# Optimization experiments

Measured on AMD Instinct MI355X. Metric: run time of the kernel, lower is better.

## Reference

```python
import jax, jax.numpy as jnp
import numpy as np
from math import sqrt

IN_DIM = 512
OUT_DIM = 512
MOD_DIM = 256
BATCH = 1024
EPS = 1e-8


def _uniform_param(key, shape, fan_in):
    # torch.rand in [0,1) then scaled to [-k, k) with k = sqrt(1/fan_in)
    k = sqrt(1.0 / fan_in)
    return jax.random.uniform(key, shape, dtype=jnp.float32, minval=-k, maxval=k)


def setup_inputs() -> dict:
    key = jax.random.key(0)
    k1, k2, k3, k4, k5, k6 = jax.random.split(key, 6)
    modulations = jax.random.normal(k1, (BATCH, MOD_DIM), dtype=jnp.float32)
    x = jax.random.normal(k2, (BATCH, IN_DIM), dtype=jnp.float32)
    weight = _uniform_param(k3, (OUT_DIM, IN_DIM), IN_DIM)      # main weight
    bias = _uniform_param(k4, (OUT_DIM,), IN_DIM)               # main bias
    # nn.Linear(modulation_dim, in_dim): weight [in_dim, mod_dim], bias [in_dim]
    mod_w = _uniform_param(k5, (IN_DIM, MOD_DIM), MOD_DIM)
    mod_b = _uniform_param(k6, (IN_DIM,), MOD_DIM)
    return {"modulations": modulations, "x": x, "weight": weight,
            "bias": bias, "mod_w": mod_w, "mod_b": mod_b}


def reference(modulations, x, weight, bias, mod_w, mod_b):
    # scales: [B, in_dim]
    scales = modulations @ mod_w.T + mod_b
    # weight_1: [B, out_dim, in_dim] = weight broadcast-scaled per sample
    w1 = weight[None, :, :] * scales[:, None, :]
    # NOTE: faithful to source: sum over axis -2 (the OUT dim), per-column L2 renorm
    w2 = w1 * jax.lax.rsqrt(jnp.sum(jnp.square(w1), axis=-2, keepdims=True) + EPS)
    # (x.unsqueeze(-2) @ w2.transpose(-2,-1)).squeeze(-2) + bias -> [B, out_dim]
    out = jnp.einsum("bi,boi->bo", x, w2) + bias
    return out
```

## Files before the change

### kernel.cpp

```cpp
#include <hip/hip_runtime.h>
#include <math.h>

#define B_DIM    1024
#define IN_DIMS  512
#define OUT_DIMS 512
#define MOD_DIM  256
#define EPS_F    1e-8f
#define SP       72

typedef __attribute__((ext_vector_type(8))) short bf16x8;
typedef __attribute__((ext_vector_type(4))) float f32x4;

__device__ __forceinline__ unsigned short f2bf(float f) {
    union { float f; unsigned u; } c; c.f = f;
    unsigned r = c.u + 0x7fffu + ((c.u >> 16) & 1u);
    return (unsigned short)(r >> 16);
}
__device__ __forceinline__ float bf2f(unsigned short h) {
    union { float f; unsigned u; } c; c.u = ((unsigned)h) << 16;
    return c.f;
}

__global__ __launch_bounds__(256) void prep_w(
    const float* __restrict__ weight, float* __restrict__ colsum,
    unsigned short* __restrict__ w_bf)
{
    __shared__ float4 sm[16][16];
    const int q = threadIdx.x & 15;
    const int r = threadIdx.x >> 4;
    const int col = blockIdx.x * 64 + q * 4;
    float4 acc = {0.f, 0.f, 0.f, 0.f};
    #pragma unroll
    for (int it = 0; it < 32; it++) {
        const int row = r + 16 * it;
        float4 v = *(const float4*)&weight[row * IN_DIMS + col];
        acc.x += v.x * v.x; acc.y += v.y * v.y;
        acc.z += v.z * v.z; acc.w += v.w * v.w;
        ushort4 h;
        h.x = f2bf(v.x); h.y = f2bf(v.y); h.z = f2bf(v.z); h.w = f2bf(v.w);
        *(ushort4*)&w_bf[row * IN_DIMS + col] = h;
    }
    sm[r][q] = acc;
    __syncthreads();
    if (threadIdx.x < 16) {
        float4 s = sm[0][threadIdx.x];
        #pragma unroll
        for (int j = 1; j < 16; j++) {
            float4 v = sm[j][threadIdx.x];
            s.x += v.x; s.y += v.y; s.z += v.z; s.w += v.w;
        }
        *(float4*)&colsum[blockIdx.x * 64 + threadIdx.x * 4] = s;
    }
}

__global__ __launch_bounds__(256) void gemm_mod(
    const float* __restrict__ A,
    const float* __restrict__ Bw,
    const float* __restrict__ mod_b,
    const float* __restrict__ x,
    const float* __restrict__ colsum,
    unsigned short* __restrict__ t_bf)
{
    __shared__ unsigned short Ah[64 * SP], Al[64 * SP], Bh[64 * SP], Bl[64 * SP];
    const int tid = threadIdx.x;
    const int m0 = blockIdx.y * 64, n0 = blockIdx.x * 64;
    const int lane = tid & 63, wv = tid >> 6;
    const int wm = (wv >> 1) * 32, wn = (wv & 1) * 32;
    const int lr = lane & 15, lq = lane >> 4;

    f32x4 acc[2][2] = {};

    for (int kt = 0; kt < MOD_DIM; kt += 64) {
        #pragma unroll
        for (int i = 0; i < 4; i++) {
            const int idx = tid + i * 256;
            const int r  = idx >> 4;
            const int k4 = (idx & 15) * 4;
            float4 va = *(const float4*)&A[(m0 + r) * MOD_DIM + kt + k4];
            ushort4 h, l;
            h.x = f2bf(va.x); l.x = f2bf(va.x - bf2f(h.x));
            h.y = f2bf(va.y); l.y = f2bf(va.y - bf2f(h.y));
            h.z = f2bf(va.z); l.z = f2bf(va.z - bf2f(h.z));
            h.w = f2bf(va.w); l.w = f2bf(va.w - bf2f(h.w));
            *(ushort4*)&Ah[r * SP + k4] = h;
            *(ushort4*)&Al[r * SP + k4] = l;
            float4 vb = *(const float4*)&Bw[(n0 + r) * MOD_DIM + kt + k4];
            h.x = f2bf(vb.x); l.x = f2bf(vb.x - bf2f(h.x));
            h.y = f2bf(vb.y); l.y = f2bf(vb.y - bf2f(h.y));
            h.z = f2bf(vb.z); l.z = f2bf(vb.z - bf2f(h.z));
            h.w = f2bf(vb.w); l.w = f2bf(vb.w - bf2f(h.w));
            *(ushort4*)&Bh[r * SP + k4] = h;
            *(ushort4*)&Bl[r * SP + k4] = l;
        }
        __syncthreads();

        #pragma unroll
        for (int kk = 0; kk < 64; kk += 32) {
            const int ko = kk + lq * 8;
            bf16x8 ah0 = *(bf16x8*)&Ah[(wm +      lr) * SP + ko];
            bf16x8 ah1 = *(bf16x8*)&Ah[(wm + 16 + lr) * SP + ko];
            bf16x8 al0 = *(bf16x8*)&Al[(wm +      lr) * SP + ko];
            bf16x8 al1 = *(bf16x8*)&Al[(wm + 16 + lr) * SP + ko];
            bf16x8 bh0 = *(bf16x8*)&Bh[(wn +      lr) * SP + ko];
            bf16x8 bh1 = *(bf16x8*)&Bh[(wn + 16 + lr) * SP + ko];
            bf16x8 bl0 = *(bf16x8*)&Bl[(wn +      lr) * SP + ko];
            bf16x8 bl1 = *(bf16x8*)&Bl[(wn + 16 + lr) * SP + ko];
            acc[0][0] = __builtin_amdgcn_mfma_f32_16x16x32_bf16(ah0, bh0, acc[0][0], 0, 0, 0);
            acc[0][1] = __builtin_amdgcn_mfma_f32_16x16x32_bf16(ah0, bh1, acc[0][1], 0, 0, 0);
            acc[1][0] = __builtin_amdgcn_mfma_f32_16x16x32_bf16(ah1, bh0, acc[1][0], 0, 0, 0);
            acc[1][1] = __builtin_amdgcn_mfma_f32_16x16x32_bf16(ah1, bh1, acc[1][1], 0, 0, 0);
            acc[0][0] = __builtin_amdgcn_mfma_f32_16x16x32_bf16(ah0, bl0, acc[0][0], 0, 0, 0);
            acc[0][1] = __builtin_amdgcn_mfma_f32_16x16x32_bf16(ah0, bl1, acc[0][1], 0, 0, 0);
            acc[1][0] = __builtin_amdgcn_mfma_f32_16x16x32_bf16(ah1, bl0, acc[1][0], 0, 0, 0);
            acc[1][1] = __builtin_amdgcn_mfma_f32_16x16x32_bf16(ah1, bl1, acc[1][1], 0, 0, 0);
            acc[0][0] = __builtin_amdgcn_mfma_f32_16x16x32_bf16(al0, bh0, acc[0][0], 0, 0, 0);
            acc[0][1] = __builtin_amdgcn_mfma_f32_16x16x32_bf16(al0, bh1, acc[0][1], 0, 0, 0);
            acc[1][0] = __builtin_amdgcn_mfma_f32_16x16x32_bf16(al1, bh0, acc[1][0], 0, 0, 0);
            acc[1][1] = __builtin_amdgcn_mfma_f32_16x16x32_bf16(al1, bh1, acc[1][1], 0, 0, 0);
        }
        __syncthreads();
    }

    #pragma unroll
    for (int i = 0; i < 2; i++) {
        #pragma unroll
        for (int j = 0; j < 2; j++) {
            const int gn = n0 + wn + 16 * j + lr;
            const float cs = colsum[gn];
            const float mb = mod_b[gn];
            #pragma unroll
            for (int rr = 0; rr < 4; rr++) {
                const int gm = m0 + wm + 16 * i + lq * 4 + rr;
                const float s = acc[i][j][rr] + mb;
                const float tv = x[gm * IN_DIMS + gn] * s * rsqrtf(s * s * cs + EPS_F);
                t_bf[gm * IN_DIMS + gn] = f2bf(tv);
            }
        }
    }
}

__global__ __launch_bounds__(256) void gemm_out(
    const unsigned short* __restrict__ A,
    const unsigned short* __restrict__ Bw,
    const float* __restrict__ bias,
    float* __restrict__ out)
{
    __shared__ unsigned short As[64 * SP], Bs[64 * SP];
    const int tid = threadIdx.x;
    const int m0 = blockIdx.y * 64, n0 = blockIdx.x * 64;
    const int lane = tid & 63, wv = tid >> 6;
    const int wm = (wv >> 1) * 32, wn = (wv & 1) * 32;
    const int lr = lane & 15, lq = lane >> 4;

    f32x4 acc[2][2] = {};

    for (int kt = 0; kt < IN_DIMS; kt += 64) {
        #pragma unroll
        for (int i = 0; i < 2; i++) {
            const int idx = tid + i * 256;
            const int r  = idx >> 3;
            const int k8 = (idx & 7) * 8;
            *(uint4*)&As[r * SP + k8] = *(const uint4*)&A [(m0 + r) * IN_DIMS + kt + k8];
            *(uint4*)&Bs[r * SP + k8] = *(const uint4*)&Bw[(n0 + r) * IN_DIMS + kt + k8];
        }
        __syncthreads();

        #pragma unroll
        for (int kk = 0; kk < 64; kk += 32) {
            const int ko = kk + lq * 8;
            bf16x8 a0 = *(bf16x8*)&As[(wm +      lr) * SP + ko];
            bf16x8 a1 = *(bf16x8*)&As[(wm + 16 + lr) * SP + ko];
            bf16x8 b0 = *(bf16x8*)&Bs[(wn +      lr) * SP + ko];
            bf16x8 b1 = *(bf16x8*)&Bs[(wn + 16 + lr) * SP + ko];
            acc[0][0] = __builtin_amdgcn_mfma_f32_16x16x32_bf16(a0, b0, acc[0][0], 0, 0, 0);
            acc[0][1] = __builtin_amdgcn_mfma_f32_16x16x32_bf16(a0, b1, acc[0][1], 0, 0, 0);
            acc[1][0] = __builtin_amdgcn_mfma_f32_16x16x32_bf16(a1, b0, acc[1][0], 0, 0, 0);
            acc[1][1] = __builtin_amdgcn_mfma_f32_16x16x32_bf16(a1, b1, acc[1][1], 0, 0, 0);
        }
        __syncthreads();
    }

    #pragma unroll
    for (int i = 0; i < 2; i++) {
        #pragma unroll
        for (int j = 0; j < 2; j++) {
            const int gn = n0 + wn + 16 * j + lr;
            const float bv = bias[gn];
            #pragma unroll
            for (int rr = 0; rr < 4; rr++) {
                const int gm = m0 + wm + 16 * i + lq * 4 + rr;
                out[gm * OUT_DIMS + gn] = acc[i][j][rr] + bv;
            }
        }
    }
}

extern "C" void kernel_launch(void* const* d_in, const int* in_sizes, int n_in,
                              void* d_out, int out_size, void* d_ws, size_t ws_size,
                              hipStream_t stream)
{
    const float* modulations = (const float*)d_in[0];
    const float* x           = (const float*)d_in[1];
    const float* weight      = (const float*)d_in[2];
    const float* bias        = (const float*)d_in[3];
    const float* mod_w       = (const float*)d_in[4];
    const float* mod_b       = (const float*)d_in[5];
    float* out = (float*)d_out;

    char* wsb = (char*)d_ws;
    float* colsum         = (float*)wsb;
    unsigned short* w_bf  = (unsigned short*)(wsb + 4096);
    unsigned short* t_bf  = (unsigned short*)(wsb + 4096 + 524288);

    prep_w<<<IN_DIMS / 64, 256, 0, stream>>>(weight, colsum, w_bf);

    gemm_mod<<<dim3(IN_DIMS / 64, B_DIM / 64), 256, 0, stream>>>(
        modulations, mod_w, mod_b, x, colsum, t_bf);

    gemm_out<<<dim3(OUT_DIMS / 64, B_DIM / 64), 256, 0, stream>>>(
        t_bf, w_bf, bias, out);
}
```

Measured before the change: 91.58 us.

## Presplit modulation operands in prep kernel and stage GEMM tiles in two large K chunks

The prep kernel now also splits mod_w and modulations into bf16 hi/lo arrays once, so gemm_mod no longer converts fp32 to split bf16 in every tile. Both GEMMs now load K in two halves: the first half goes to LDS, and the second half is prefetched into registers while the first is computed. This cuts the number of barriers and overlaps global loads with MFMA work. The cost is larger LDS use (64KB in gemm_mod, 64KB in gemm_out), unpadded row strides that may cause bank conflicts, more workspace traffic, and higher register pressure that may lower occupancy.

New measurement: 99.96 us. 1.09x slower.

```diff
diff --git a/kernel.cpp b/kernel.cpp
--- a/kernel.cpp
+++ b/kernel.cpp
@@ -6,7 +6,6 @@
 #define OUT_DIMS 512
 #define MOD_DIM  256
 #define EPS_F    1e-8f
-#define SP       72
 
 typedef __attribute__((ext_vector_type(8))) short bf16x8;
 typedef __attribute__((ext_vector_type(4))) float f32x4;
@@ -20,91 +19,139 @@
     union { float f; unsigned u; } c; c.u = ((unsigned)h) << 16;
     return c.f;
 }
-
-__global__ __launch_bounds__(256) void prep_w(
-    const float* __restrict__ weight, float* __restrict__ colsum,
-    unsigned short* __restrict__ w_bf)
-{
-    __shared__ float4 sm[16][16];
-    const int q = threadIdx.x & 15;
-    const int r = threadIdx.x >> 4;
-    const int col = blockIdx.x * 64 + q * 4;
-    float4 acc = {0.f, 0.f, 0.f, 0.f};
-    #pragma unroll
-    for (int it = 0; it < 32; it++) {
-        const int row = r + 16 * it;
-        float4 v = *(const float4*)&weight[row * IN_DIMS + col];
-        acc.x += v.x * v.x; acc.y += v.y * v.y;
-        acc.z += v.z * v.z; acc.w += v.w * v.w;
-        ushort4 h;
-        h.x = f2bf(v.x); h.y = f2bf(v.y); h.z = f2bf(v.z); h.w = f2bf(v.w);
-        *(ushort4*)&w_bf[row * IN_DIMS + col] = h;
-    }
-    sm[r][q] = acc;
-    __syncthreads();
-    if (threadIdx.x < 16) {
-        float4 s = sm[0][threadIdx.x];
-        #pragma unroll
-        for (int j = 1; j < 16; j++) {
-            float4 v = sm[j][threadIdx.x];
-            s.x += v.x; s.y += v.y; s.z += v.z; s.w += v.w;
-        }
-        *(float4*)&colsum[blockIdx.x * 64 + threadIdx.x * 4] = s;
+__device__ __forceinline__ void split4(float4 v, ushort4& h, ushort4& l) {
+    h.x = f2bf(v.x); l.x = f2bf(v.x - bf2f(h.x));
+    h.y = f2bf(v.y); l.y = f2bf(v.y - bf2f(h.y));
+    h.z = f2bf(v.z); l.z = f2bf(v.z - bf2f(h.z));
+    h.w = f2bf(v.w); l.w = f2bf(v.w - bf2f(h.w));
+}
+
+__global__ __launch_bounds__(256) void prep(
+    const float* __restrict__ weight, const float* __restrict__ mod_w,
+    const float* __restrict__ mods,
+    float* __restrict__ colsum, unsigned short* __restrict__ w_bf,
+    unsigned short* __restrict__ mwh, unsigned short* __restrict__ mwl,
+    unsigned short* __restrict__ mh,  unsigned short* __restrict__ ml)
+{
+    const int b = blockIdx.x, tid = threadIdx.x;
+    if (b < 8) {
+        __shared__ float4 sm[16][16];
+        const int q = tid & 15, r = tid >> 4;
+        const int col = b * 64 + q * 4;
+        float4 acc = {0.f, 0.f, 0.f, 0.f};
+        #pragma unroll
+        for (int it = 0; it < 32; it++) {
+            const int row = r + 16 * it;
+            float4 v = *(const float4*)&weight[row * IN_DIMS + col];
+            acc.x += v.x * v.x; acc.y += v.y * v.y;
+            acc.z += v.z * v.z; acc.w += v.w * v.w;
+            ushort4 h;
+            h.x = f2bf(v.x); h.y = f2bf(v.y); h.z = f2bf(v.z); h.w = f2bf(v.w);
+            *(ushort4*)&w_bf[row * IN_DIMS + col] = h;
+        }
+        sm[r][q] = acc;
+        __syncthreads();
+        if (tid < 16) {
+            float4 s = sm[0][tid];
+            #pragma unroll
+            for (int j = 1; j < 16; j++) {
+                float4 v = sm[j][tid];
+                s.x += v.x; s.y += v.y; s.z += v.z; s.w += v.w;
+            }
+            *(float4*)&colsum[b * 64 + tid * 4] = s;
+        }
+    } else if (b < 16) {
+        const int rb = b - 8;
+        #pragma unroll
+        for (int i = 0; i < 16; i++) {
+            const int id = tid + i * 256;
+            const int r = rb * 64 + (id >> 6);
+            const int c = (id & 63) * 4;
+            float4 v = *(const float4*)&mod_w[r * MOD_DIM + c];
+            ushort4 h, l; split4(v, h, l);
+            *(ushort4*)&mwh[r * MOD_DIM + c] = h;
+            *(ushort4*)&mwl[r * MOD_DIM + c] = l;
+        }
+    } else {
+        const int rb = b - 16;
+        #pragma unroll
+        for (int i = 0; i < 8; i++) {
+            const int id = tid + i * 256;
+            const int r = rb * 32 + (id >> 6);
+            const int c = (id & 63) * 4;
+            float4 v = *(const float4*)&mods[r * MOD_DIM + c];
+            ushort4 h, l; split4(v, h, l);
+            *(ushort4*)&mh[r * MOD_DIM + c] = h;
+            *(ushort4*)&ml[r * MOD_DIM + c] = l;
+        }
     }
 }
 
 __global__ __launch_bounds__(256) void gemm_mod(
-    const float* __restrict__ A,
-    const float* __restrict__ Bw,
-    const float* __restrict__ mod_b,
-    const float* __restrict__ x,
-    const float* __restrict__ colsum,
-    unsigned short* __restrict__ t_bf)
-{
-    __shared__ unsigned short Ah[64 * SP], Al[64 * SP], Bh[64 * SP], Bl[64 * SP];
+    const unsigned short* __restrict__ Amh, const unsigned short* __restrict__ Aml,
+    const unsigned short* __restrict__ Bmh, const unsigned short* __restrict__ Bml,
+    const float* __restrict__ mod_b, const float* __restrict__ x,
+    const float* __restrict__ colsum, unsigned short* __restrict__ t_bf)
+{
+    __shared__ unsigned short Ah[64 * 128], Al[64 * 128], Bh[64 * 128], Bl[64 * 128];
     const int tid = threadIdx.x;
     const int m0 = blockIdx.y * 64, n0 = blockIdx.x * 64;
     const int lane = tid & 63, wv = tid >> 6;
     const int wm = (wv >> 1) * 32, wn = (wv & 1) * 32;
     const int lr = lane & 15, lq = lane >> 4;
 
+    int sr[4], sc[4];
+    #pragma unroll
+    for (int i = 0; i < 4; i++) { int id = tid + i * 256; sr[i] = id >> 4; sc[i] = (id & 15) * 8; }
+
+    uint4 gah[4], gal[4], gbh[4], gbl[4];
+    #pragma unroll
+    for (int i = 0; i < 4; i++) {
+        gah[i] = *(const uint4*)&Amh[(m0 + sr[i]) * MOD_DIM + sc[i]];
+        gal[i] = *(const uint4*)&Aml[(m0 + sr[i]) * MOD_DIM + sc[i]];
+        gbh[i] = *(const uint4*)&Bmh[(n0 + sr[i]) * MOD_DIM + sc[i]];
+        gbl[i] = *(const uint4*)&Bml[(n0 + sr[i]) * MOD_DIM + sc[i]];
+    }
+    #pragma unroll
+    for (int i = 0; i < 4; i++) {
+        *(uint4*)&Ah[sr[i] * 128 + sc[i]] = gah[i];
+        *(uint4*)&Al[sr[i] * 128 + sc[i]] = gal[i];
+        *(uint4*)&Bh[sr[i] * 128 + sc[i]] = gbh[i];
+        *(uint4*)&Bl[sr[i] * 128 + sc[i]] = gbl[i];
+    }
+    #pragma unroll
+    for (int i = 0; i < 4; i++) {
+        gah[i] = *(const uint4*)&Amh[(m0 + sr[i]) * MOD_DIM + 128 + sc[i]];
+        gal[i] = *(const uint4*)&Aml[(m0 + sr[i]) * MOD_DIM + 128 + sc[i]];
+        gbh[i] = *(const uint4*)&Bmh[(n0 + sr[i]) * MOD_DIM + 128 + sc[i]];
+        gbl[i] = *(const uint4*)&Bml[(n0 + sr[i]) * MOD_DIM + 128 + sc[i]];
+    }
+
     f32x4 acc[2][2] = {};
-
-    for (int kt = 0; kt < MOD_DIM; kt += 64) {
-        #pragma unroll
-        for (int i = 0; i < 4; i++) {
-            const int idx = tid + i * 256;
-            const int r  = idx >> 4;
-            const int k4 = (idx & 15) * 4;
-            float4 va = *(const float4*)&A[(m0 + r) * MOD_DIM + kt + k4];
-            ushort4 h, l;
-            h.x = f2bf(va.x); l.x = f2bf(va.x - bf2f(h.x));
-            h.y = f2bf(va.y); l.y = f2bf(va.y - bf2f(h.y));
-            h.z = f2bf(va.z); l.z = f2bf(va.z - bf2f(h.z));
-            h.w = f2bf(va.w); l.w = f2bf(va.w - bf2f(h.w));
-            *(ushort4*)&Ah[r * SP + k4] = h;
-            *(ushort4*)&Al[r * SP + k4] = l;
-            float4 vb = *(const float4*)&Bw[(n0 + r) * MOD_DIM + kt + k4];
-            h.x = f2bf(vb.x); l.x = f2bf(vb.x - bf2f(h.x));
-            h.y = f2bf(vb.y); l.y = f2bf(vb.y - bf2f(h.y));
-            h.z = f2bf(vb.z); l.z = f2bf(vb.z - bf2f(h.z));
-            h.w = f2bf(vb.w); l.w = f2bf(vb.w - bf2f(h.w));
-            *(ushort4*)&Bh[r * SP + k4] = h;
-            *(ushort4*)&Bl[r * SP + k4] = l;
-        }
+    #pragma unroll
+    for (int it = 0; it < 2; it++) {
         __syncthreads();
-
-        #pragma unroll
-        for (int kk = 0; kk < 64; kk += 32) {
+        if (it == 1) {
+            #pragma unroll
+            for (int i = 0; i < 4; i++) {
+                *(uint4*)&Ah[sr[i] * 128 + sc[i]] = gah[i];
+                *(uint4*)&Al[sr[i] * 128 + sc[i]] = gal[i];
+                *(uint4*)&Bh[sr[i] * 128 + sc[i]] = gbh[i];
+                *(uint4*)&Bl[sr[i] * 128 + sc[i]] = gbl[i];
+            }
+            __syncthreads();
+        }
+        #pragma unroll
+        for (int kk = 0; kk < 128; kk += 32) {
             const int ko = kk + lq * 8;
-            bf16x8 ah0 = *(bf16x8*)&Ah[(wm +      lr) * SP + ko];
-            bf16x8 ah1 = *(bf16x8*)&Ah[(wm + 16 + lr) * SP + ko];
-            bf16x8 al0 = *(bf16x8*)&Al[(wm +      lr) * SP + ko];
-            bf16x8 al1 = *(bf16x8*)&Al[(wm + 16 + lr) * SP + ko];
-            bf16x8 bh0 = *(bf16x8*)&Bh[(wn +      lr) * SP + ko];
-            bf16x8 bh1 = *(bf16x8*)&Bh[(wn + 16 + lr) * SP + ko];
-            bf16x8 bl0 = *(bf16x8*)&Bl[(wn +      lr) * SP + ko];
-            bf16x8 bl1 = *(bf16x8*)&Bl[(wn + 16 + lr) * SP + ko];
+            bf16x8 ah0 = *(bf16x8*)&Ah[(wm +      lr) * 128 + ko];
+            bf16x8 ah1 = *(bf16x8*)&Ah[(wm + 16 + lr) * 128 + ko];
+            bf16x8 al0 = *(bf16x8*)&Al[(wm +      lr) * 128 + ko];
+            bf16x8 al1 = *(bf16x8*)&Al[(wm + 16 + lr) * 128 + ko];
+            bf16x8 bh0 = *(bf16x8*)&Bh[(wn +      lr) * 128 + ko];
+            bf16x8 bh1 = *(bf16x8*)&Bh[(wn + 16 + lr) * 128 + ko];
+            bf16x8 bl0 = *(bf16x8*)&Bl[(wn +      lr) * 128 + ko];
+            bf16x8 bl1 = *(bf16x8*)&Bl[(wn + 16 + lr) * 128 + ko];
             acc[0][0] = __builtin_amdgcn_mfma_f32_16x16x32_bf16(ah0, bh0, acc[0][0], 0, 0, 0);
             acc[0][1] = __builtin_amdgcn_mfma_f32_16x16x32_bf16(ah0, bh1, acc[0][1], 0, 0, 0);
             acc[1][0] = __builtin_amdgcn_mfma_f32_16x16x32_bf16(ah1, bh0, acc[1][0], 0, 0, 0);
@@ -118,7 +165,6 @@
             acc[1][0] = __builtin_amdgcn_mfma_f32_16x16x32_bf16(al1, bh0, acc[1][0], 0, 0, 0);
             acc[1][1] = __builtin_amdgcn_mfma_f32_16x16x32_bf16(al1, bh1, acc[1][1], 0, 0, 0);
         }
-        __syncthreads();
     }
 
     #pragma unroll
@@ -142,42 +188,60 @@
 __global__ __launch_bounds__(256) void gemm_out(
     const unsigned short* __restrict__ A,
     const unsigned short* __restrict__ Bw,
-    const float* __restrict__ bias,
-    float* __restrict__ out)
-{
-    __shared__ unsigned short As[64 * SP], Bs[64 * SP];
+    const float* __restrict__ bias, float* __restrict__ out)
+{
+    __shared__ unsigned short As[64 * 256], Bs[64 * 256];
     const int tid = threadIdx.x;
     const int m0 = blockIdx.y * 64, n0 = blockIdx.x * 64;
     const int lane = tid & 63, wv = tid >> 6;
     const int wm = (wv >> 1) * 32, wn = (wv & 1) * 32;
     const int lr = lane & 15, lq = lane >> 4;
 
+    int sr[8], sc[8];
+    #pragma unroll
+    for (int i = 0; i < 8; i++) { int id = tid + i * 256; sr[i] = id >> 5; sc[i] = (id & 31) * 8; }
+
+    uint4 ga[8], gb[8];
+    #pragma unroll
+    for (int i = 0; i < 8; i++) {
+        ga[i] = *(const uint4*)&A [(m0 + sr[i]) * IN_DIMS + sc[i]];
+        gb[i] = *(const uint4*)&Bw[(n0 + sr[i]) * IN_DIMS + sc[i]];
+    }
+    #pragma unroll
+    for (int i = 0; i < 8; i++) {
+        *(uint4*)&As[sr[i] * 256 + sc[i]] = ga[i];
+        *(uint4*)&Bs[sr[i] * 256 + sc[i]] = gb[i];
+    }
+    #pragma unroll
+    for (int i = 0; i < 8; i++) {
+        ga[i] = *(const uint4*)&A [(m0 + sr[i]) * IN_DIMS + 256 + sc[i]];
+        gb[i] = *(const uint4*)&Bw[(n0 + sr[i]) * IN_DIMS + 256 + sc[i]];
+    }
+
     f32x4 acc[2][2] = {};
-
-    for (int kt = 0; kt < IN_DIMS; kt += 64) {
-        #pragma unroll
-        for (int i = 0; i < 2; i++) {
-            const int idx = tid + i * 256;
-            const int r  = idx >> 3;
-            const int k8 = (idx & 7) * 8;
-            *(uint4*)&As[r * SP + k8] = *(const uint4*)&A [(m0 + r) * IN_DIMS + kt + k8];
-            *(uint4*)&Bs[r * SP + k8] = *(const uint4*)&Bw[(n0 + r) * IN_DIMS + kt + k8];
-        }
+    #pragma unroll
+    for (int it = 0; it < 2; it++) {
         __syncthreads();
-
-        #pragma unroll
-        for (int kk = 0; kk < 64; kk += 32) {
+        if (it == 1) {
+            #pragma unroll
+            for (int i = 0; i < 8; i++) {
+                *(uint4*)&As[sr[i] * 256 + sc[i]] = ga[i];
+                *(uint4*)&Bs[sr[i] * 256 + sc[i]] = gb[i];
+            }
+            __syncthreads();
+        }
+        #pragma unroll
+        for (int kk = 0; kk < 256; kk += 32) {
             const int ko = kk + lq * 8;
-            bf16x8 a0 = *(bf16x8*)&As[(wm +      lr) * SP + ko];
-            bf16x8 a1 = *(bf16x8*)&As[(wm + 16 + lr) * SP + ko];
-            bf16x8 b0 = *(bf16x8*)&Bs[(wn +      lr) * SP + ko];
-            bf16x8 b1 = *(bf16x8*)&Bs[(wn + 16 + lr) * SP + ko];
+            bf16x8 a0 = *(bf16x8*)&As[(wm +      lr) * 256 + ko];
+            bf16x8 a1 = *(bf16x8*)&As[(wm + 16 + lr) * 256 + ko];
+            bf16x8 b0 = *(bf16x8*)&Bs[(wn +      lr) * 256 + ko];
+            bf16x8 b1 = *(bf16x8*)&Bs[(wn + 16 + lr) * 256 + ko];
             acc[0][0] = __builtin_amdgcn_mfma_f32_16x16x32_bf16(a0, b0, acc[0][0], 0, 0, 0);
             acc[0][1] = __builtin_amdgcn_mfma_f32_16x16x32_bf16(a0, b1, acc[0][1], 0, 0, 0);
             acc[1][0] = __builtin_amdgcn_mfma_f32_16x16x32_bf16(a1, b0, acc[1][0], 0, 0, 0);
             acc[1][1] = __builtin_amdgcn_mfma_f32_16x16x32_bf16(a1, b1, acc[1][1], 0, 0, 0);
         }
-        __syncthreads();
     }
 
     #pragma unroll
@@ -208,14 +272,19 @@
     float* out = (float*)d_out;
 
     char* wsb = (char*)d_ws;
-    float* colsum         = (float*)wsb;
-    unsigned short* w_bf  = (unsigned short*)(wsb + 4096);
-    unsigned short* t_bf  = (unsigned short*)(wsb + 4096 + 524288);
-
-    prep_w<<<IN_DIMS / 64, 256, 0, stream>>>(weight, colsum, w_bf);
+    float* colsum        = (float*)wsb;
+    unsigned short* w_bf = (unsigned short*)(wsb + 4096);
+    unsigned short* t_bf = (unsigned short*)(wsb + 4096 + 524288);
+    unsigned short* mwh  = (unsigned short*)(wsb + 4096 + 524288 + 1048576);
+    unsigned short* mwl  = (unsigned short*)(wsb + 4096 + 524288 + 1048576 + 262144);
+    unsigned short* mh   = (unsigned short*)(wsb + 4096 + 524288 + 1048576 + 524288);
+    unsigned short* ml   = (unsigned short*)(wsb + 4096 + 524288 + 1048576 + 524288 + 524288);
+
+    prep<<<48, 256, 0, stream>>>(weight, mod_w, modulations,
+                                 colsum, w_bf, mwh, mwl, mh, ml);
 
     gemm_mod<<<dim3(IN_DIMS / 64, B_DIM / 64), 256, 0, stream>>>(
-        modulations, mod_w, mod_b, x, colsum, t_bf);
+        mh, ml, mwh, mwl, mod_b, x, colsum, t_bf);
 
     gemm_out<<<dim3(OUT_DIMS / 64, B_DIM / 64), 256, 0, stream>>>(
         t_bf, w_bf, bias, out);
```

## Fold weight prep into both GEMM kernels and stage full-K tiles in LDS

Applied to the files above, without the earlier changes.

Removes the separate prep_w kernel. Each k1_mod block now recomputes its own column sums of weight, and k2_out converts fp32 weight to bf16 on the fly. Both GEMMs switch to 32x64 tiles, so each uses 256 blocks, and they load the whole K extent into LDS once instead of looping over K-tiles. This drops one launch and the workspace round trip for w_bf, at the cost of redundant weight reads (32x per column block), more LDS per block that may lower occupancy, and no overlap between loads and MFMA work.

After: 77.44 us. 15.4% less time.

```diff
diff --git a/kernel.cpp b/kernel.cpp
--- a/kernel.cpp
+++ b/kernel.cpp
@@ -6,7 +6,6 @@
 #define OUT_DIMS 512
 #define MOD_DIM  256
 #define EPS_F    1e-8f
-#define SP       72
 
 typedef __attribute__((ext_vector_type(8))) short bf16x8;
 typedef __attribute__((ext_vector_type(4))) float f32x4;
@@ -21,176 +20,166 @@
     return c.f;
 }
 
-__global__ __launch_bounds__(256) void prep_w(
-    const float* __restrict__ weight, float* __restrict__ colsum,
-    unsigned short* __restrict__ w_bf)
-{
-    __shared__ float4 sm[16][16];
-    const int q = threadIdx.x & 15;
-    const int r = threadIdx.x >> 4;
-    const int col = blockIdx.x * 64 + q * 4;
-    float4 acc = {0.f, 0.f, 0.f, 0.f};
-    #pragma unroll
-    for (int it = 0; it < 32; it++) {
-        const int row = r + 16 * it;
-        float4 v = *(const float4*)&weight[row * IN_DIMS + col];
-        acc.x += v.x * v.x; acc.y += v.y * v.y;
-        acc.z += v.z * v.z; acc.w += v.w * v.w;
-        ushort4 h;
-        h.x = f2bf(v.x); h.y = f2bf(v.y); h.z = f2bf(v.z); h.w = f2bf(v.w);
-        *(ushort4*)&w_bf[row * IN_DIMS + col] = h;
-    }
-    sm[r][q] = acc;
-    __syncthreads();
-    if (threadIdx.x < 16) {
-        float4 s = sm[0][threadIdx.x];
-        #pragma unroll
-        for (int j = 1; j < 16; j++) {
-            float4 v = sm[j][threadIdx.x];
-            s.x += v.x; s.y += v.y; s.z += v.z; s.w += v.w;
-        }
-        *(float4*)&colsum[blockIdx.x * 64 + threadIdx.x * 4] = s;
-    }
-}
-
-__global__ __launch_bounds__(256) void gemm_mod(
-    const float* __restrict__ A,
-    const float* __restrict__ Bw,
+#define LP1 264
+__global__ __launch_bounds__(256) void k1_mod(
+    const float* __restrict__ mods,
+    const float* __restrict__ mod_w,
     const float* __restrict__ mod_b,
+    const float* __restrict__ weight,
     const float* __restrict__ x,
-    const float* __restrict__ colsum,
     unsigned short* __restrict__ t_bf)
 {
-    __shared__ unsigned short Ah[64 * SP], Al[64 * SP], Bh[64 * SP], Bl[64 * SP];
+    __shared__ unsigned short Ah[32 * LP1], Al[32 * LP1];
+    __shared__ unsigned short Bh[64 * LP1], Bl[64 * LP1];
+    __shared__ float4 csm[16][16];
+    __shared__ float colsum_s[64];
+
     const int tid = threadIdx.x;
-    const int m0 = blockIdx.y * 64, n0 = blockIdx.x * 64;
+    const int n0 = blockIdx.x * 64;
+    const int m0 = blockIdx.y * 32;
     const int lane = tid & 63, wv = tid >> 6;
-    const int wm = (wv >> 1) * 32, wn = (wv & 1) * 32;
+    const int wm = (wv >> 1) * 16, wn = (wv & 1) * 32;
     const int lr = lane & 15, lq = lane >> 4;
 
-    f32x4 acc[2][2] = {};
-
-    for (int kt = 0; kt < MOD_DIM; kt += 64) {
-        #pragma unroll
-        for (int i = 0; i < 4; i++) {
-            const int idx = tid + i * 256;
-            const int r  = idx >> 4;
-            const int k4 = (idx & 15) * 4;
-            float4 va = *(const float4*)&A[(m0 + r) * MOD_DIM + kt + k4];
-            ushort4 h, l;
-            h.x = f2bf(va.x); l.x = f2bf(va.x - bf2f(h.x));
-            h.y = f2bf(va.y); l.y = f2bf(va.y - bf2f(h.y));
-            h.z = f2bf(va.z); l.z = f2bf(va.z - bf2f(h.z));
-            h.w = f2bf(va.w); l.w = f2bf(va.w - bf2f(h.w));
-            *(ushort4*)&Ah[r * SP + k4] = h;
-            *(ushort4*)&Al[r * SP + k4] = l;
-            float4 vb = *(const float4*)&Bw[(n0 + r) * MOD_DIM + kt + k4];
-            h.x = f2bf(vb.x); l.x = f2bf(vb.x - bf2f(h.x));
-            h.y = f2bf(vb.y); l.y = f2bf(vb.y - bf2f(h.y));
-            h.z = f2bf(vb.z); l.z = f2bf(vb.z - bf2f(h.z));
-            h.w = f2bf(vb.w); l.w = f2bf(vb.w - bf2f(h.w));
-            *(ushort4*)&Bh[r * SP + k4] = h;
-            *(ushort4*)&Bl[r * SP + k4] = l;
-        }
-        __syncthreads();
-
-        #pragma unroll
-        for (int kk = 0; kk < 64; kk += 32) {
-            const int ko = kk + lq * 8;
-            bf16x8 ah0 = *(bf16x8*)&Ah[(wm +      lr) * SP + ko];
-            bf16x8 ah1 = *(bf16x8*)&Ah[(wm + 16 + lr) * SP + ko];
-            bf16x8 al0 = *(bf16x8*)&Al[(wm +      lr) * SP + ko];
-            bf16x8 al1 = *(bf16x8*)&Al[(wm + 16 + lr) * SP + ko];
-            bf16x8 bh0 = *(bf16x8*)&Bh[(wn +      lr) * SP + ko];
-            bf16x8 bh1 = *(bf16x8*)&Bh[(wn + 16 + lr) * SP + ko];
-            bf16x8 bl0 = *(bf16x8*)&Bl[(wn +      lr) * SP + ko];
-            bf16x8 bl1 = *(bf16x8*)&Bl[(wn + 16 + lr) * SP + ko];
-            acc[0][0] = __builtin_amdgcn_mfma_f32_16x16x32_bf16(ah0, bh0, acc[0][0], 0, 0, 0);
-            acc[0][1] = __builtin_amdgcn_mfma_f32_16x16x32_bf16(ah0, bh1, acc[0][1], 0, 0, 0);
-            acc[1][0] = __builtin_amdgcn_mfma_f32_16x16x32_bf16(ah1, bh0, acc[1][0], 0, 0, 0);
-            acc[1][1] = __builtin_amdgcn_mfma_f32_16x16x32_bf16(ah1, bh1, acc[1][1], 0, 0, 0);
-            acc[0][0] = __builtin_amdgcn_mfma_f32_16x16x32_bf16(ah0, bl0, acc[0][0], 0, 0, 0);
-            acc[0][1] = __builtin_amdgcn_mfma_f32_16x16x32_bf16(ah0, bl1, acc[0][1], 0, 0, 0);
-            acc[1][0] = __builtin_amdgcn_mfma_f32_16x16x32_bf16(ah1, bl0, acc[1][0], 0, 0, 0);
-            acc[1][1] = __builtin_amdgcn_mfma_f32_16x16x32_bf16(ah1, bl1, acc[1][1], 0, 0, 0);
-            acc[0][0] = __builtin_amdgcn_mfma_f32_16x16x32_bf16(al0, bh0, acc[0][0], 0, 0, 0);
-            acc[0][1] = __builtin_amdgcn_mfma_f32_16x16x32_bf16(al0, bh1, acc[0][1], 0, 0, 0);
-            acc[1][0] = __builtin_amdgcn_mfma_f32_16x16x32_bf16(al1, bh0, acc[1][0], 0, 0, 0);
-            acc[1][1] = __builtin_amdgcn_mfma_f32_16x16x32_bf16(al1, bh1, acc[1][1], 0, 0, 0);
-        }
-        __syncthreads();
-    }
-
-    #pragma unroll
-    for (int i = 0; i < 2; i++) {
-        #pragma unroll
-        for (int j = 0; j < 2; j++) {
-            const int gn = n0 + wn + 16 * j + lr;
-            const float cs = colsum[gn];
-            const float mb = mod_b[gn];
-            #pragma unroll
-            for (int rr = 0; rr < 4; rr++) {
-                const int gm = m0 + wm + 16 * i + lq * 4 + rr;
-                const float s = acc[i][j][rr] + mb;
-                const float tv = x[gm * IN_DIMS + gn] * s * rsqrtf(s * s * cs + EPS_F);
-                t_bf[gm * IN_DIMS + gn] = f2bf(tv);
-            }
-        }
-    }
-}
-
-__global__ __launch_bounds__(256) void gemm_out(
-    const unsigned short* __restrict__ A,
-    const unsigned short* __restrict__ Bw,
+    #pragma unroll
+    for (int i = 0; i < 8; i++) {
+        const int id = tid + i * 256;
+        const int r = id >> 6, c4 = id & 63;
+        float4 v = *(const float4*)&mods[(m0 + r) * MOD_DIM + c4 * 4];
+        ushort4 h, l;
+        h.x = f2bf(v.x); l.x = f2bf(v.x - bf2f(h.x));
+        h.y = f2bf(v.y); l.y = f2bf(v.y - bf2f(h.y));
+        h.z = f2bf(v.z); l.z = f2bf(v.z - bf2f(h.z));
+        h.w = f2bf(v.w); l.w = f2bf(v.w - bf2f(h.w));
+        *(ushort4*)&Ah[r * LP1 + c4 * 4] = h;
+        *(ushort4*)&Al[r * LP1 + c4 * 4] = l;
+    }
+    #pragma unroll
+    for (int i = 0; i < 16; i++) {
+        const int id = tid + i * 256;
+        const int r = id >> 6, c4 = id & 63;
+        float4 v = *(const float4*)&mod_w[(n0 + r) * MOD_DIM + c4 * 4];
+        ushort4 h, l;
+        h.x = f2bf(v.x); l.x = f2bf(v.x - bf2f(h.x));
+        h.y = f2bf(v.y); l.y = f2bf(v.y - bf2f(h.y));
+        h.z = f2bf(v.z); l.z = f2bf(v.z - bf2f(h.z));
+        h.w = f2bf(v.w); l.w = f2bf(v.w - bf2f(h.w));
+        *(ushort4*)&Bh[r * LP1 + c4 * 4] = h;
+        *(ushort4*)&Bl[r * LP1 + c4 * 4] = l;
+    }
+
+    {
+        const int c4 = tid & 15, rr = tid >> 4;
+        float4 acc = {0.f, 0.f, 0.f, 0.f};
+        #pragma unroll
+        for (int it = 0; it < 32; it++) {
+            const int row = rr + 16 * it;
+            float4 v = *(const float4*)&weight[row * IN_DIMS + n0 + c4 * 4];
+            acc.x += v.x * v.x; acc.y += v.y * v.y;
+            acc.z += v.z * v.z; acc.w += v.w * v.w;
+        }
+        csm[rr][c4] = acc;
+    }
+    __syncthreads();
+    if (tid < 16) {
+        float4 s = csm[0][tid];
+        #pragma unroll
+        for (int j = 1; j < 16; j++) {
+            float4 v = csm[j][tid];
+            s.x += v.x; s.y += v.y; s.z += v.z; s.w += v.w;
+        }
+        *(float4*)&colsum_s[tid * 4] = s;
+    }
+
+    f32x4 acc[2] = {};
+    #pragma unroll
+    for (int kk = 0; kk < 256; kk += 32) {
+        const int ko = kk + lq * 8;
+        bf16x8 ah = *(bf16x8*)&Ah[(wm + lr) * LP1 + ko];
+        bf16x8 al = *(bf16x8*)&Al[(wm + lr) * LP1 + ko];
+        bf16x8 bh0 = *(bf16x8*)&Bh[(wn +      lr) * LP1 + ko];
+        bf16x8 bh1 = *(bf16x8*)&Bh[(wn + 16 + lr) * LP1 + ko];
+        bf16x8 bl0 = *(bf16x8*)&Bl[(wn +      lr) * LP1 + ko];
+        bf16x8 bl1 = *(bf16x8*)&Bl[(wn + 16 + lr) * LP1 + ko];
+        acc[0] = __builtin_amdgcn_mfma_f32_16x16x32_bf16(ah, bh0, acc[0], 0, 0, 0);
+        acc[1] = __builtin_amdgcn_mfma_f32_16x16x32_bf16(ah, bh1, acc[1], 0, 0, 0);
+        acc[0] = __builtin_amdgcn_mfma_f32_16x16x32_bf16(ah, bl0, acc[0], 0, 0, 0);
+        acc[1] = __builtin_amdgcn_mfma_f32_16x16x32_bf16(ah, bl1, acc[1], 0, 0, 0);
+        acc[0] = __builtin_amdgcn_mfma_f32_16x16x32_bf16(al, bh0, acc[0], 0, 0, 0);
+        acc[1] = __builtin_amdgcn_mfma_f32_16x16x32_bf16(al, bh1, acc[1], 0, 0, 0);
+    }
+    __syncthreads();
+
+    #pragma unroll
+    for (int j = 0; j < 2; j++) {
+        const int ln = wn + 16 * j + lr;
+        const int gn = n0 + ln;
+        const float cs = colsum_s[ln];
+        const float mb = mod_b[gn];
+        #pragma unroll
+        for (int rr = 0; rr < 4; rr++) {
+            const int gm = m0 + wm + lq * 4 + rr;
+            const float s = acc[j][rr] + mb;
+            const float tv = x[gm * IN_DIMS + gn] * s * rsqrtf(s * s * cs + EPS_F);
+            t_bf[gm * IN_DIMS + gn] = f2bf(tv);
+        }
+    }
+}
+
+#define LP2 536
+__global__ __launch_bounds__(256) void k2_out(
+    const unsigned short* __restrict__ t_bf,
+    const float* __restrict__ weight,
     const float* __restrict__ bias,
     float* __restrict__ out)
 {
-    __shared__ unsigned short As[64 * SP], Bs[64 * SP];
+    __shared__ unsigned short As[32 * LP2];
+    __shared__ unsigned short Bs[64 * LP2];
+
     const int tid = threadIdx.x;
-    const int m0 = blockIdx.y * 64, n0 = blockIdx.x * 64;
+    const int n0 = blockIdx.x * 64;
+    const int m0 = blockIdx.y * 32;
     const int lane = tid & 63, wv = tid >> 6;
-    const int wm = (wv >> 1) * 32, wn = (wv & 1) * 32;
+    const int wm = (wv >> 1) * 16, wn = (wv & 1) * 32;
     const int lr = lane & 15, lq = lane >> 4;
 
-    f32x4 acc[2][2] = {};
-
-    for (int kt = 0; kt < IN_DIMS; kt += 64) {
-        #pragma unroll
-        for (int i = 0; i < 2; i++) {
-            const int idx = tid + i * 256;
-            const int r  = idx >> 3;
-            const int k8 = (idx & 7) * 8;
-            *(uint4*)&As[r * SP + k8] = *(const uint4*)&A [(m0 + r) * IN_DIMS + kt + k8];
-            *(uint4*)&Bs[r * SP + k8] = *(const uint4*)&Bw[(n0 + r) * IN_DIMS + kt + k8];
-        }
-        __syncthreads();
-
-        #pragma unroll
-        for (int kk = 0; kk < 64; kk += 32) {
-            const int ko = kk + lq * 8;
-            bf16x8 a0 = *(bf16x8*)&As[(wm +      lr) * SP + ko];
-            bf16x8 a1 = *(bf16x8*)&As[(wm + 16 + lr) * SP + ko];
-            bf16x8 b0 = *(bf16x8*)&Bs[(wn +      lr) * SP + ko];
-            bf16x8 b1 = *(bf16x8*)&Bs[(wn + 16 + lr) * SP + ko];
-            acc[0][0] = __builtin_amdgcn_mfma_f32_16x16x32_bf16(a0, b0, acc[0][0], 0, 0, 0);
-            acc[0][1] = __builtin_amdgcn_mfma_f32_16x16x32_bf16(a0, b1, acc[0][1], 0, 0, 0);
-            acc[1][0] = __builtin_amdgcn_mfma_f32_16x16x32_bf16(a1, b0, acc[1][0], 0, 0, 0);
-            acc[1][1] = __builtin_amdgcn_mfma_f32_16x16x32_bf16(a1, b1, acc[1][1], 0, 0, 0);
-        }
-        __syncthreads();
-    }
-
-    #pragma unroll
-    for (int i = 0; i < 2; i++) {
-        #pragma unroll
-        for (int j = 0; j < 2; j++) {
-            const int gn = n0 + wn + 16 * j + lr;
-            const float bv = bias[gn];
-            #pragma unroll
-            for (int rr = 0; rr < 4; rr++) {
-                const int gm = m0 + wm + 16 * i + lq * 4 + rr;
-                out[gm * OUT_DIMS + gn] = acc[i][j][rr] + bv;
-            }
+    #pragma unroll
+    for (int i = 0; i < 8; i++) {
+        const int id = tid + i * 256;
+        const int r = id >> 6, c8 = id & 63;
+        *(uint4*)&As[r * LP2 + c8 * 8] =
+            *(const uint4*)&t_bf[(m0 + r) * IN_DIMS + c8 * 8];
+    }
+    #pragma unroll
+    for (int i = 0; i < 32; i++) {
+        const int id = tid + i * 256;
+        const int r = id >> 7, c4 = id & 127;
+        float4 v = *(const float4*)&weight[(n0 + r) * IN_DIMS + c4 * 4];
+        ushort4 h;
+        h.x = f2bf(v.x); h.y = f2bf(v.y); h.z = f2bf(v.z); h.w = f2bf(v.w);
+        *(ushort4*)&Bs[r * LP2 + c4 * 4] = h;
+    }
+    __syncthreads();
+
+    f32x4 acc[2] = {};
+    #pragma unroll
+    for (int kk = 0; kk < 512; kk += 32) {
+        const int ko = kk + lq * 8;
+        bf16x8 a  = *(bf16x8*)&As[(wm + lr) * LP2 + ko];
+        bf16x8 b0 = *(bf16x8*)&Bs[(wn +      lr) * LP2 + ko];
+        bf16x8 b1 = *(bf16x8*)&Bs[(wn + 16 + lr) * LP2 + ko];
+        acc[0] = __builtin_amdgcn_mfma_f32_16x16x32_bf16(a, b0, acc[0], 0, 0, 0);
+        acc[1] = __builtin_amdgcn_mfma_f32_16x16x32_bf16(a, b1, acc[1], 0, 0, 0);
+    }
+
+    #pragma unroll
+    for (int j = 0; j < 2; j++) {
+        const int gn = n0 + wn + 16 * j + lr;
+        const float bv = bias[gn];
+        #pragma unroll
+        for (int rr = 0; rr < 4; rr++) {
+            const int gm = m0 + wm + lq * 4 + rr;
+            out[gm * OUT_DIMS + gn] = acc[j][rr] + bv;
         }
     }
 }
@@ -207,16 +196,11 @@
     const float* mod_b       = (const float*)d_in[5];
     float* out = (float*)d_out;
 
-    char* wsb = (char*)d_ws;
-    float* colsum         = (float*)wsb;
-    unsigned short* w_bf  = (unsigned short*)(wsb + 4096);
-    unsigned short* t_bf  = (unsigned short*)(wsb + 4096 + 524288);
-
-    prep_w<<<IN_DIMS / 64, 256, 0, stream>>>(weight, colsum, w_bf);
-
-    gemm_mod<<<dim3(IN_DIMS / 64, B_DIM / 64), 256, 0, stream>>>(
-        modulations, mod_w, mod_b, x, colsum, t_bf);
-
-    gemm_out<<<dim3(OUT_DIMS / 64, B_DIM / 64), 256, 0, stream>>>(
-        t_bf, w_bf, bias, out);
-}
+    unsigned short* t_bf = (unsigned short*)d_ws;
+
+    k1_mod<<<dim3(8, 32), 256, 0, stream>>>(
+        modulations, mod_w, mod_b, weight, x, t_bf);
+
+    k2_out<<<dim3(8, 32), 256, 0, stream>>>(
+        t_bf, weight, bias, out);
+}
```
